# Performance work log

Measured on AMD Instinct MI355X. Metric: run time of the kernel, lower is better.

The kernel has to match this reference:

```python
import jax, jax.numpy as jnp
from jax import lax
import numpy as np

B, C_IN, DIMS, NW = 8, 64, 64, 8
T, H, W = 16, 56, 56
HID = C_IN // 4 + 1
EPS = 1e-5


def setup_inputs() -> dict:
    key = jax.random.key(0)
    ks = jax.random.split(key, 8)
    fan_in = C_IN * 27
    x = jax.random.normal(ks[0], (B, C_IN, T, H, W), dtype=jnp.float32)
    weights = jax.random.normal(ks[1], (NW, DIMS, C_IN, 3, 3, 3), dtype=jnp.float32) * np.sqrt(2.0 / fan_in)
    biases = jax.random.normal(ks[2], (NW, DIMS), dtype=jnp.float32)
    W1 = jax.random.normal(ks[3], (HID, C_IN), dtype=jnp.float32) * np.sqrt(1.0 / C_IN)
    b1 = jnp.zeros((HID,), dtype=jnp.float32)
    W2 = jax.random.normal(ks[4], (NW, HID), dtype=jnp.float32) * np.sqrt(1.0 / HID)
    b2 = jnp.zeros((NW,), dtype=jnp.float32)
    gamma = jnp.ones((DIMS,), dtype=jnp.float32)
    beta = jnp.zeros((DIMS,), dtype=jnp.float32)
    return {"x": x, "weights": weights, "biases": biases, "W1": W1, "b1": b1,
            "W2": W2, "b2": b2, "gamma": gamma, "beta": beta, "epochs_num": 5}


def reference(x, weights, biases, W1, b1, W2, b2, gamma, beta, epochs_num):
    # temperature schedule (epochs_num is a Python int)
    tau = 30.0 - 2.9 * epochs_num if epochs_num < 10 else 1.0
    # global max pool over (T,H,W) -> (B, C_in); sum over singleton dims is identity
    pooled = jnp.max(x, axis=(2, 3, 4))
    h = jax.nn.relu(pooled @ W1.T + b1)
    logits = h @ W2.T + b2
    phi = jax.nn.softmax(logits / tau, axis=1)  # (B, NW)
    # synthesize per-sample kernels and biases
    dyn_w = jnp.einsum('bn,noidhw->boidhw', phi, weights)  # (B, DIMS, C_in, 3,3,3)
    dyn_b = phi @ biases  # (B, DIMS)
    # per-sample conv3d (equivalent to grouped conv with groups=B)
    def conv1(xi, wi):
        return lax.conv_general_dilated(
            xi[None], wi, window_strides=(1, 1, 1), padding='SAME',
            dimension_numbers=('NCDHW', 'OIDHW', 'NCDHW'))[0]
    y = jax.vmap(conv1)(x, dyn_w) + dyn_b[:, :, None, None, None]
    # BatchNorm3d (training mode: batch statistics, biased var) + ReLU
    mean = jnp.mean(y, axis=(0, 2, 3, 4))
    var = jnp.var(y, axis=(0, 2, 3, 4))
    yn = (y - mean[None, :, None, None, None]) * lax.rsqrt(var + EPS)[None, :, None, None, None]
    yn = yn * gamma[None, :, None, None, None] + beta[None, :, None, None, None]
    return jax.nn.relu(yn)
```

## Files before the change

### kernel.cpp

```cpp
#include <hip/hip_runtime.h>
#include <hip/hip_bf16.h>

#define B_   8
#define CIN  64
#define DIMS 64
#define NW   8
#define T_   16
#define H_   56
#define W_   56
#define HID  17
#define THW  (T_*H_*W_)
#define HW   (H_*W_)
#define NPC  401408
#define EPS  1e-5f
#define PROWS 348

typedef __bf16 bf16x8 __attribute__((ext_vector_type(8)));
typedef float f32x4 __attribute__((ext_vector_type(4)));

#define OFF_XT     0
#define OFF_AT     51380224
#define OFF_POOLED 53149696
#define OFF_CHSUM  53151744
#define OFF_CHSQ   53152000
#define OFF_PHI    53152256
#define OFF_DYNB   53152512
#define OFF_SCALE  53154560
#define OFF_SHIFT  53154816
#define OFF_Y      53155072
#define WS_NEED_BF16Y (OFF_Y + 51380224)

__device__ __forceinline__ unsigned short f2bf(float f) {
    unsigned int u = __float_as_uint(f);
    u += 0x7fffu + ((u >> 16) & 1u);
    return (unsigned short)(u >> 16);
}
__device__ __forceinline__ float bf2f(unsigned short u) {
    return __uint_as_float(((unsigned int)u) << 16);
}
__device__ __forceinline__ unsigned int fenc(float f) {
    unsigned int b = __float_as_uint(f);
    return (b & 0x80000000u) ? ~b : (b | 0x80000000u);
}
__device__ __forceinline__ float fdec(unsigned int e) {
    return (e & 0x80000000u) ? __uint_as_float(e & 0x7fffffffu) : __uint_as_float(~e);
}

__device__ __forceinline__ float waveRedSum(float v) {
    #pragma unroll
    for (int o = 32; o > 0; o >>= 1) v += __shfl_down(v, o);
    return v;
}

__global__ __launch_bounds__(256) void xpose_kernel(const float* __restrict__ x,
                                                    unsigned short* __restrict__ xT,
                                                    unsigned int* __restrict__ pooled_u) {
    __shared__ float tile[CIN * W_];
    const int h = blockIdx.x, t = blockIdx.y, b = blockIdx.z;
    const int tid = threadIdx.x;
    {
        const int w = tid & 63, cg = tid >> 6;
        if (w < W_) {
            const size_t base = ((size_t)(b * CIN) * T_ + t) * HW + h * W_ + w;
            #pragma unroll
            for (int k = 0; k < 16; ++k) {
                const int c = cg * 16 + k;
                tile[c * W_ + w] = x[base + (size_t)c * (T_ * HW)];
            }
        }
    }
    __syncthreads();
    {
        const int w = tid >> 2, cq = tid & 3;
        if (w < W_) {
            unsigned int pk[8];
            #pragma unroll
            for (int kk = 0; kk < 8; ++kk) {
                const float f0 = tile[(cq * 16 + kk * 2) * W_ + w];
                const float f1 = tile[(cq * 16 + kk * 2 + 1) * W_ + w];
                pk[kk] = (unsigned int)f2bf(f0) | ((unsigned int)f2bf(f1) << 16);
            }
            unsigned short* dst = xT + ((((size_t)b * T_ + t) * H_ + h) * W_ + w) * CIN + cq * 16;
            *reinterpret_cast<uint4*>(dst)     = make_uint4(pk[0], pk[1], pk[2], pk[3]);
            *reinterpret_cast<uint4*>(dst + 8) = make_uint4(pk[4], pk[5], pk[6], pk[7]);
        }
    }
    if (tid < CIN) {
        float m = -3.4e38f;
        #pragma unroll 8
        for (int w = 0; w < W_; ++w) m = fmaxf(m, tile[tid * W_ + w]);
        atomicMax(&pooled_u[b * CIN + tid], fenc(m));
    }
}

__global__ __launch_bounds__(256) void mlp_kernel(const unsigned int* __restrict__ pooled_u,
                                                  const float* __restrict__ W1,
                                                  const float* __restrict__ b1,
                                                  const float* __restrict__ W2,
                                                  const float* __restrict__ b2,
                                                  const float* __restrict__ biases,
                                                  const void* __restrict__ epochs,
                                                  float* __restrict__ phi_out,
                                                  float* __restrict__ dynb) {
    __shared__ float pool_s[B_ * CIN];
    __shared__ float h_s[B_ * HID];
    __shared__ float lg_s[B_ * NW];
    __shared__ float phi_s[B_ * NW];
    const int tid = threadIdx.x;
    for (int i = tid; i < B_ * CIN; i += 256) pool_s[i] = fdec(pooled_u[i]);
    __syncthreads();
    if (tid < B_ * HID) {
        const int bb = tid / HID, j = tid % HID;
        float acc = b1[j];
        #pragma unroll
        for (int c = 0; c < CIN; ++c) acc += pool_s[bb * CIN + c] * W1[j * CIN + c];
        h_s[tid] = fmaxf(acc, 0.0f);
    }
    __syncthreads();
    if (tid < B_ * NW) {
        const int bb = tid >> 3, n = tid & 7;
        float acc = b2[n];
        #pragma unroll
        for (int j = 0; j < HID; ++j) acc += h_s[bb * HID + j] * W2[n * HID + j];
        lg_s[tid] = acc;
    }
    __syncthreads();
    if (tid < B_) {
        int e = ((const int*)epochs)[0];
        if (e < 0 || e > 1000000) e = (int)(((const float*)epochs)[0]);
        const float tau = (e < 10) ? (30.0f - 2.9f * (float)e) : 1.0f;
        float mx = -3.4e38f;
        #pragma unroll
        for (int n = 0; n < NW; ++n) mx = fmaxf(mx, lg_s[tid * NW + n]);
        float ex[NW], s = 0.0f;
        #pragma unroll
        for (int n = 0; n < NW; ++n) { ex[n] = expf((lg_s[tid * NW + n] - mx) / tau); s += ex[n]; }
        const bool ok = (s >= 1.0f) && (s < 1e37f);
        const float inv = ok ? (1.0f / s) : 0.0f;
        #pragma unroll
        for (int n = 0; n < NW; ++n) phi_s[tid * NW + n] = ok ? (ex[n] * inv) : 0.125f;
    }
    __syncthreads();
    if (tid < B_ * NW) phi_out[tid] = phi_s[tid];
    for (int idx = tid; idx < B_ * DIMS; idx += 256) {
        const int bb = idx >> 6, o = idx & 63;
        float a = 0.0f;
        #pragma unroll
        for (int n = 0; n < NW; ++n) a += phi_s[bb * NW + n] * biases[n * DIMS + o];
        dynb[idx] = a;
    }
}

__global__ __launch_bounds__(256) void awgen_kernel(const float* __restrict__ weights,
                                                    const float* __restrict__ phi,
                                                    unsigned short* __restrict__ At2) {
    const int b = blockIdx.x >> 5, oc = blockIdx.x & 31;
    const int o0 = oc * 2;
    __shared__ float ph[NW];
    if (threadIdx.x < NW) ph[threadIdx.x] = phi[b * NW + threadIdx.x];
    __syncthreads();
    const float4* w4 = reinterpret_cast<const float4*>(weights);
    for (int j = threadIdx.x; j < 864; j += 256) {
        f32x4 a = (f32x4){0.f, 0.f, 0.f, 0.f};
        #pragma unroll
        for (int n = 0; n < NW; ++n) {
            const float4 wv = w4[(size_t)(n * 64 + o0) * 432 + j];
            a[0] += ph[n] * wv.x;
            a[1] += ph[n] * wv.y;
            a[2] += ph[n] * wv.z;
            a[3] += ph[n] * wv.w;
        }
        #pragma unroll
        for (int k = 0; k < 4; ++k) {
            const int idx = j * 4 + k;
            const int oo = idx / 1728;
            const int rem = idx - oo * 1728;
            const int i = rem / 27;
            const int tap = rem - i * 27;
            const int o = o0 + oo;
            const int m = o >> 4, colv = o & 15;
            const int ks = i >> 5, kgv = (i >> 3) & 3, jj = i & 7;
            const size_t dst = (size_t)(b * 27 + tap) * 4096
                             + ((((ks * 4 + m) * 64) + kgv * 16 + colv) * 8 + jj);
            At2[dst] = f2bf(a[k]);
        }
    }
}

template<int BF16Y>
__global__ __launch_bounds__(256) void conv_kernel(const unsigned short* __restrict__ xT,
                                                   const unsigned short* __restrict__ At2,
                                                   const float* __restrict__ dynb,
                                                   float* __restrict__ yf,
                                                   unsigned short* __restrict__ yb) {
    __shared__ __align__(16) unsigned char xs[PROWS * 128];
    const int swz = (blockIdx.x & 7) * 224 + (blockIdx.x >> 3);
    const int b = swz / 224;
    const int rem = swz - b * 224;
    const int t = rem / 14, hg = rem - t * 14;
    const int tid = threadIdx.x;
    const int wave = tid >> 6, lane = tid & 63;
    const int col = lane & 15, kg = lane >> 4;
    const int hr = wave;
    const int h = hg * 4 + hr;

    for (int idx = tid; idx < PROWS * 8; idx += 256) {
        const int p = idx >> 3;
        const int hh = p / 58, ww = p - hh * 58;
        const int hha = hg * 4 + hh - 1;
        if (hha < 0 || hha >= H_ || ww == 0 || ww == 57)
            *reinterpret_cast<uint4*>(&xs[idx * 16]) = make_uint4(0u, 0u, 0u, 0u);
    }

    f32x4 acc[4][4];
    #pragma unroll
    for (int m = 0; m < 4; ++m)
        #pragma unroll
        for (int n = 0; n < 4; ++n) acc[m][n] = (f32x4){0.f, 0.f, 0.f, 0.f};

    const int sub = lane >> 3, q = lane & 7;

    for (int kd = 0; kd < 3; ++kd) {
        const int td = t + kd - 1;
        if (td < 0 || td >= T_) continue;
        __syncthreads();
        for (int item = wave; item < 42; item += 4) {
            const int hh = item / 7, qv = item - hh * 7;
            const int hha = hg * 4 + hh - 1;
            if (hha < 0 || hha >= H_) continue;
            const int p0 = hh * 58 + 1 + qv * 8;
            const int p = p0 + sub;
            const int w = qv * 8 + sub;
            const int qq = q ^ (p & 7);
            const unsigned short* src = xT
                + ((((size_t)b * T_ + td) * H_ + hha) * W_ + w) * CIN + qq * 8;
            __builtin_amdgcn_global_load_lds(
                (const __attribute__((address_space(1))) unsigned int*)(const void*)src,
                (__attribute__((address_space(3))) unsigned int*)(void*)&xs[p0 * 128],
                16, 0, 0);
        }
        asm volatile("s_waitcnt vmcnt(0)" ::: "memory");
        __syncthreads();
        #pragma unroll
        for (int kh = 0; kh < 3; ++kh) {
            #pragma unroll
            for (int kw = 0; kw < 3; ++kw) {
                const int tap = kd * 9 + kh * 3 + kw;
                const unsigned short* ap = At2 + (size_t)(b * 27 + tap) * 4096;
                bf16x8 afr[4][2], bfr[4][2];
                #pragma unroll
                for (int ks = 0; ks < 2; ++ks)
                    #pragma unroll
                    for (int m = 0; m < 4; ++m)
                        afr[m][ks] = *reinterpret_cast<const bf16x8*>(
                            ap + (((ks * 4 + m) * 64) + lane) * 8);
                #pragma unroll
                for (int n = 0; n < 4; ++n) {
                    int ww = n * 16 + col + kw;
                    if (ww > 57) ww = 57;
                    const int p = (hr + kh) * 58 + ww;
                    #pragma unroll
                    for (int ks = 0; ks < 2; ++ks) {
                        const int slot = (ks * 4 + kg) ^ (p & 7);
                        bfr[n][ks] = *reinterpret_cast<const bf16x8*>(&xs[p * 128 + slot * 16]);
                    }
                }
                #pragma unroll
                for (int ks = 0; ks < 2; ++ks)
                    #pragma unroll
                    for (int m = 0; m < 4; ++m)
                        #pragma unroll
                        for (int n = 0; n < 4; ++n)
                            acc[m][n] = __builtin_amdgcn_mfma_f32_16x16x32_bf16(
                                afr[m][ks], bfr[n][ks], acc[m][n], 0, 0, 0);
            }
        }
    }

    #pragma unroll
    for (int m = 0; m < 4; ++m) {
        #pragma unroll
        for (int r = 0; r < 4; ++r) {
            const int o = m * 16 + kg * 4 + r;
            const float db = dynb[b * DIMS + o];
            const size_t base = ((size_t)(b * DIMS + o) * T_ + t) * HW + h * W_;
            #pragma unroll
            for (int n = 0; n < 4; ++n) {
                const int w = n * 16 + col;
                if (w < W_) {
                    const float v = acc[m][n][r] + db;
                    if (BF16Y) yb[base + w] = f2bf(v);
                    else       yf[base + w] = v;
                }
            }
        }
    }
}

__global__ __launch_bounds__(256) void stats_f32_kernel(const float* __restrict__ y,
                                                        float* __restrict__ chsum,
                                                        float* __restrict__ chsq) {
    const int bo = blockIdx.x;
    const int o = bo & 63;
    const float4* src = reinterpret_cast<const float4*>(y + (size_t)bo * THW);
    float s = 0.0f, qq = 0.0f;
    for (int idx = threadIdx.x; idx < THW / 4; idx += 256) {
        float4 v = src[idx];
        s += v.x + v.y + v.z + v.w;
        qq += v.x * v.x + v.y * v.y + v.z * v.z + v.w * v.w;
    }
    s = waveRedSum(s);
    qq = waveRedSum(qq);
    __shared__ float ls[4], lq[4];
    const int wave = threadIdx.x >> 6, lane = threadIdx.x & 63;
    if (lane == 0) { ls[wave] = s; lq[wave] = qq; }
    __syncthreads();
    if (threadIdx.x == 0) {
        atomicAdd(&chsum[o], ls[0] + ls[1] + ls[2] + ls[3]);
        atomicAdd(&chsq[o],  lq[0] + lq[1] + lq[2] + lq[3]);
    }
}

__global__ __launch_bounds__(256) void stats_bf16_kernel(const unsigned short* __restrict__ yb,
                                                         float* __restrict__ chsum,
                                                         float* __restrict__ chsq) {
    const int bo = blockIdx.x;
    const int o = bo & 63;
    const uint4* src = reinterpret_cast<const uint4*>(yb + (size_t)bo * THW);
    float s = 0.0f, qq = 0.0f;
    for (int idx = threadIdx.x; idx < THW / 8; idx += 256) {
        uint4 v = src[idx];
        unsigned int vv[4] = {v.x, v.y, v.z, v.w};
        #pragma unroll
        for (int k = 0; k < 4; ++k) {
            float f0 = __uint_as_float((vv[k] & 0xffffu) << 16);
            float f1 = __uint_as_float(vv[k] & 0xffff0000u);
            s += f0 + f1;
            qq += f0 * f0 + f1 * f1;
        }
    }
    s = waveRedSum(s);
    qq = waveRedSum(qq);
    __shared__ float ls[4], lq[4];
    const int wave = threadIdx.x >> 6, lane = threadIdx.x & 63;
    if (lane == 0) { ls[wave] = s; lq[wave] = qq; }
    __syncthreads();
    if (threadIdx.x == 0) {
        atomicAdd(&chsum[o], ls[0] + ls[1] + ls[2] + ls[3]);
        atomicAdd(&chsq[o],  lq[0] + lq[1] + lq[2] + lq[3]);
    }
}

__global__ void fin_kernel(const float* __restrict__ chsum, const float* __restrict__ chsq,
                           const float* __restrict__ gamma, const float* __restrict__ beta,
                           float* __restrict__ scale, float* __restrict__ shift,
                           const unsigned int* __restrict__ pooled_u,
                           const float* __restrict__ phi,
                           int hostflags, float* __restrict__ out) {
    const int o = threadIdx.x;
    if (o < DIMS) {
        const float inv = 1.0f / (float)NPC;
        const float mean = chsum[o] * inv;
        const float var = chsq[o] * inv - mean * mean;
        const bool ok = (fabsf(mean) < 1e30f) && (var >= 0.0f) && (var < 1e30f);
        const float rstd = ok ? rsqrtf(var + EPS) : 0.0f;
        const float s = gamma[o] * rstd;
        scale[o] = ok ? s : 0.0f;
        shift[o] = ok ? (beta[o] - mean * s) : 0.69f;
    }
    if (o == 0) {
        int D = 32;
        const float p0 = fdec(pooled_u[0]);
        if (isfinite(p0) && fabsf(p0) > 1e-20f) D += 16;
        float sp = 0.0f, mp = 0.0f;
        for (int n = 0; n < NW; ++n) { sp += phi[n]; mp = fmaxf(mp, phi[n]); }
        if (fabsf(sp - 1.0f) < 0.01f) D += 32;
        float sq = 0.0f;
        for (int c = 0; c < DIMS; ++c) sq += chsq[c];
        if (sq > 1e-10f) D += 128;
        if (mp > 0.25f) D += 256;
        D += hostflags;
        if (D != 32 + 16 + 32 + 128) out[0] = (float)D;
    }
}

__global__ __launch_bounds__(256) void norm_f32_kernel(float* __restrict__ y,
                                                       const float* __restrict__ scale,
                                                       const float* __restrict__ shift) {
    const int bo = blockIdx.x >> 2, qq = blockIdx.x & 3;
    const int o = bo & 63;
    const float s = scale[o], sh = shift[o];
    float4* buf = reinterpret_cast<float4*>(y + (size_t)bo * THW) + qq * (THW / 16);
    for (int idx = threadIdx.x; idx < THW / 16; idx += 256) {
        float4 v = buf[idx];
        v.x = fmaxf(v.x * s + sh, 0.0f);
        v.y = fmaxf(v.y * s + sh, 0.0f);
        v.z = fmaxf(v.z * s + sh, 0.0f);
        v.w = fmaxf(v.w * s + sh, 0.0f);
        buf[idx] = v;
    }
}

__global__ __launch_bounds__(256) void norm_bf16_kernel(const unsigned short* __restrict__ yb,
                                                        const float* __restrict__ scale,
                                                        const float* __restrict__ shift,
                                                        float* __restrict__ out) {
    const int bo = blockIdx.x >> 2, qq = blockIdx.x & 3;
    const int o = bo & 63;
    const float s = scale[o], sh = shift[o];
    const uint4* src = reinterpret_cast<const uint4*>(yb + (size_t)bo * THW) + qq * (THW / 32);
    float4* dst = reinterpret_cast<float4*>(out + (size_t)bo * THW) + qq * (THW / 16);
    for (int idx = threadIdx.x; idx < THW / 32; idx += 256) {
        uint4 v = src[idx];
        unsigned int vv[4] = {v.x, v.y, v.z, v.w};
        float4 r0, r1;
        float* rp[2] = {&r0.x, &r1.x};
        #pragma unroll
        for (int k = 0; k < 4; ++k) {
            float f0 = __uint_as_float((vv[k] & 0xffffu) << 16);
            float f1 = __uint_as_float(vv[k] & 0xffff0000u);
            rp[k >> 1][(k & 1) * 2]     = fmaxf(f0 * s + sh, 0.0f);
            rp[k >> 1][(k & 1) * 2 + 1] = fmaxf(f1 * s + sh, 0.0f);
        }
        dst[idx * 2]     = r0;
        dst[idx * 2 + 1] = r1;
    }
}

extern "C" void kernel_launch(void* const* d_in, const int* in_sizes, int n_in,
                              void* d_out, int out_size, void* d_ws, size_t ws_size,
                              hipStream_t stream) {
    const float* x       = (const float*)d_in[0];
    const float* weights = (const float*)d_in[1];
    const float* biases  = (const float*)d_in[2];
    const float* W1      = (const float*)d_in[3];
    const float* b1      = (const float*)d_in[4];
    const float* W2      = (const float*)d_in[5];
    const float* b2      = (const float*)d_in[6];
    const float* gamma   = (const float*)d_in[7];
    const float* beta    = (const float*)d_in[8];
    const void*  epochs  = (const void*)d_in[9];

    float* out = (float*)d_out;
    char* ws = (char*)d_ws;
    unsigned short* xT   = (unsigned short*)(ws + OFF_XT);
    unsigned short* At2  = (unsigned short*)(ws + OFF_AT);
    unsigned int* pooled = (unsigned int*)(ws + OFF_POOLED);
    float* chsum  = (float*)(ws + OFF_CHSUM);
    float* chsq   = (float*)(ws + OFF_CHSQ);
    float* phi    = (float*)(ws + OFF_PHI);
    float* dynb   = (float*)(ws + OFF_DYNB);
    float* scale  = (float*)(ws + OFF_SCALE);
    float* shift  = (float*)(ws + OFF_SHIFT);
    unsigned short* ybf  = (unsigned short*)(ws + OFF_Y);

    const bool bf16y = (ws_size >= (size_t)WS_NEED_BF16Y);

    int hflags = 0;
    {
        const int expect[10] = {25690112, 884736, 512, 1088, 17, 136, 8, 64, 64, 1};
        if (n_in != 10) hflags |= 512;
        else {
            for (int i = 0; i < 10; ++i)
                if (in_sizes[i] != expect[i]) { hflags |= 512; break; }
        }
        if (out_size != 25690112) hflags |= 1024;
        if (ws_size < 53155072) hflags |= 2048;
    }

    hipMemsetAsync(ws + OFF_POOLED, 0, 2560, stream);

    xpose_kernel<<<dim3(H_, T_, B_), 256, 0, stream>>>(x, xT, pooled);
    mlp_kernel<<<1, 256, 0, stream>>>(pooled, W1, b1, W2, b2, biases, epochs, phi, dynb);
    awgen_kernel<<<256, 256, 0, stream>>>(weights, phi, At2);
    if (bf16y) {
        conv_kernel<1><<<1792, 256, 0, stream>>>(xT, At2, dynb, out, ybf);
        stats_bf16_kernel<<<B_ * DIMS, 256, 0, stream>>>(ybf, chsum, chsq);
        fin_kernel<<<1, 64, 0, stream>>>(chsum, chsq, gamma, beta, scale, shift,
                                         pooled, phi, hflags, out);
        norm_bf16_kernel<<<2048, 256, 0, stream>>>(ybf, scale, shift, out);
    } else {
        conv_kernel<0><<<1792, 256, 0, stream>>>(xT, At2, dynb, out, nullptr);
        stats_f32_kernel<<<B_ * DIMS, 256, 0, stream>>>(out, chsum, chsq);
        fin_kernel<<<1, 64, 0, stream>>>(chsum, chsq, gamma, beta, scale, shift,
                                         pooled, phi, hflags, out);
        norm_f32_kernel<<<2048, 256, 0, stream>>>(out, scale, shift);
    }
}
```

Baseline: 235.2 us.

## Split conv tiles along width into two halves to double block count

The conv kernel's output tile is halved along W: each block now covers 4 rows × 28 columns instead of the full 56-wide row, and the grid doubles to 3584 blocks. The shared-memory halo shrinks to 34-wide rows, the padding logic is reworked, and block-to-batch mapping changes so the batch index comes from the low bits. The goal is better load balance and occupancy on the GPU's compute units, using less LDS per block. In exchange, each block loads more halo per output and reuses each A-fragment load for half as many MFMAs, which adds weight-fetch traffic.

```diff
diff --git a/kernel.cpp b/kernel.cpp
--- a/kernel.cpp
+++ b/kernel.cpp
@@ -13,7 +13,8 @@
 #define HW   (H_*W_)
 #define NPC  401408
 #define EPS  1e-5f
-#define PROWS 348
+#define WWID 34
+#define PROWS_W (6*WWID)
 
 typedef __bf16 bf16x8 __attribute__((ext_vector_type(8)));
 typedef float f32x4 __attribute__((ext_vector_type(4)));
@@ -193,53 +194,57 @@
                                                    const float* __restrict__ dynb,
                                                    float* __restrict__ yf,
                                                    unsigned short* __restrict__ yb) {
-    __shared__ __align__(16) unsigned char xs[PROWS * 128];
-    const int swz = (blockIdx.x & 7) * 224 + (blockIdx.x >> 3);
-    const int b = swz / 224;
-    const int rem = swz - b * 224;
-    const int t = rem / 14, hg = rem - t * 14;
+    __shared__ __align__(16) unsigned char xs[PROWS_W * 128];
+    const int b = blockIdx.x & 7;
+    const int rem = blockIdx.x >> 3;
+    const int t = rem / 28;
+    const int r2 = rem - t * 28;
+    const int hg = r2 >> 1, wb = r2 & 1;
     const int tid = threadIdx.x;
     const int wave = tid >> 6, lane = tid & 63;
     const int col = lane & 15, kg = lane >> 4;
     const int hr = wave;
     const int h = hg * 4 + hr;
 
-    for (int idx = tid; idx < PROWS * 8; idx += 256) {
-        const int p = idx >> 3;
-        const int hh = p / 58, ww = p - hh * 58;
-        const int hha = hg * 4 + hh - 1;
-        if (hha < 0 || hha >= H_ || ww == 0 || ww == 57)
-            *reinterpret_cast<uint4*>(&xs[idx * 16]) = make_uint4(0u, 0u, 0u, 0u);
-    }
-
-    f32x4 acc[4][4];
+    for (int idx = tid; idx < PROWS_W * 8; idx += 256)
+        *reinterpret_cast<uint4*>(&xs[idx * 16]) = make_uint4(0u, 0u, 0u, 0u);
+
+    f32x4 acc[4][2];
     #pragma unroll
     for (int m = 0; m < 4; ++m)
         #pragma unroll
-        for (int n = 0; n < 4; ++n) acc[m][n] = (f32x4){0.f, 0.f, 0.f, 0.f};
+        for (int n = 0; n < 2; ++n) acc[m][n] = (f32x4){0.f, 0.f, 0.f, 0.f};
 
     const int sub = lane >> 3, q = lane & 7;
+    const int ww_s = (wb == 0) ? 1 : 0;
 
     for (int kd = 0; kd < 3; ++kd) {
         const int td = t + kd - 1;
         if (td < 0 || td >= T_) continue;
         __syncthreads();
-        for (int item = wave; item < 42; item += 4) {
-            const int hh = item / 7, qv = item - hh * 7;
+        for (int item = wave; item < 24; item += 4) {
+            const int hh = item >> 2, qv = item & 3;
             const int hha = hg * 4 + hh - 1;
             if (hha < 0 || hha >= H_) continue;
-            const int p0 = hh * 58 + 1 + qv * 8;
+            const int p0 = hh * WWID + ww_s + qv * 8;
             const int p = p0 + sub;
-            const int w = qv * 8 + sub;
+            const int ww = ww_s + qv * 8 + sub;
+            int w_in = wb * 28 + ww - 1;
+            if (w_in > 55) w_in = 55;
             const int qq = q ^ (p & 7);
             const unsigned short* src = xT
-                + ((((size_t)b * T_ + td) * H_ + hha) * W_ + w) * CIN + qq * 8;
+                + ((((size_t)b * T_ + td) * H_ + hha) * W_ + w_in) * CIN + qq * 8;
             __builtin_amdgcn_global_load_lds(
                 (const __attribute__((address_space(1))) unsigned int*)(const void*)src,
                 (__attribute__((address_space(3))) unsigned int*)(void*)&xs[p0 * 128],
                 16, 0, 0);
         }
         asm volatile("s_waitcnt vmcnt(0)" ::: "memory");
+        if (wb && wave == 3 && lane < 48) {
+            const int hh = lane >> 3, qz = lane & 7;
+            *reinterpret_cast<uint4*>(&xs[(hh * WWID + 29) * 128 + qz * 16]) =
+                make_uint4(0u, 0u, 0u, 0u);
+        }
         __syncthreads();
         #pragma unroll
         for (int kh = 0; kh < 3; ++kh) {
@@ -247,7 +252,7 @@
             for (int kw = 0; kw < 3; ++kw) {
                 const int tap = kd * 9 + kh * 3 + kw;
                 const unsigned short* ap = At2 + (size_t)(b * 27 + tap) * 4096;
-                bf16x8 afr[4][2], bfr[4][2];
+                bf16x8 afr[4][2], bfr[2][2];
                 #pragma unroll
                 for (int ks = 0; ks < 2; ++ks)
                     #pragma unroll
@@ -255,10 +260,10 @@
                         afr[m][ks] = *reinterpret_cast<const bf16x8*>(
                             ap + (((ks * 4 + m) * 64) + lane) * 8);
                 #pragma unroll
-                for (int n = 0; n < 4; ++n) {
+                for (int n = 0; n < 2; ++n) {
                     int ww = n * 16 + col + kw;
-                    if (ww > 57) ww = 57;
-                    const int p = (hr + kh) * 58 + ww;
+                    if (ww > 29) ww = 29;
+                    const int p = (hr + kh) * WWID + ww;
                     #pragma unroll
                     for (int ks = 0; ks < 2; ++ks) {
                         const int slot = (ks * 4 + kg) ^ (p & 7);
@@ -270,7 +275,7 @@
                     #pragma unroll
                     for (int m = 0; m < 4; ++m)
                         #pragma unroll
-                        for (int n = 0; n < 4; ++n)
+                        for (int n = 0; n < 2; ++n)
                             acc[m][n] = __builtin_amdgcn_mfma_f32_16x16x32_bf16(
                                 afr[m][ks], bfr[n][ks], acc[m][n], 0, 0, 0);
             }
@@ -283,14 +288,14 @@
         for (int r = 0; r < 4; ++r) {
             const int o = m * 16 + kg * 4 + r;
             const float db = dynb[b * DIMS + o];
-            const size_t base = ((size_t)(b * DIMS + o) * T_ + t) * HW + h * W_;
+            const size_t base = ((size_t)(b * DIMS + o) * T_ + t) * HW + h * W_ + wb * 28;
             #pragma unroll
-            for (int n = 0; n < 4; ++n) {
-                const int w = n * 16 + col;
-                if (w < W_) {
+            for (int n = 0; n < 2; ++n) {
+                const int wc = n * 16 + col;
+                if (wc < 28) {
                     const float v = acc[m][n][r] + db;
-                    if (BF16Y) yb[base + w] = f2bf(v);
-                    else       yf[base + w] = v;
+                    if (BF16Y) yb[base + wc] = f2bf(v);
+                    else       yf[base + wc] = v;
                 }
             }
         }
@@ -474,13 +479,13 @@
     mlp_kernel<<<1, 256, 0, stream>>>(pooled, W1, b1, W2, b2, biases, epochs, phi, dynb);
     awgen_kernel<<<256, 256, 0, stream>>>(weights, phi, At2);
     if (bf16y) {
-        conv_kernel<1><<<1792, 256, 0, stream>>>(xT, At2, dynb, out, ybf);
+        conv_kernel<1><<<3584, 256, 0, stream>>>(xT, At2, dynb, out, ybf);
         stats_bf16_kernel<<<B_ * DIMS, 256, 0, stream>>>(ybf, chsum, chsq);
         fin_kernel<<<1, 64, 0, stream>>>(chsum, chsq, gamma, beta, scale, shift,
                                          pooled, phi, hflags, out);
         norm_bf16_kernel<<<2048, 256, 0, stream>>>(ybf, scale, shift, out);
     } else {
-        conv_kernel<0><<<1792, 256, 0, stream>>>(xT, At2, dynb, out, nullptr);
+        conv_kernel<0><<<3584, 256, 0, stream>>>(xT, At2, dynb, out, nullptr);
         stats_f32_kernel<<<B_ * DIMS, 256, 0, stream>>>(out, chsum, chsq);
         fin_kernel<<<1, 64, 0, stream>>>(chsum, chsq, gamma, beta, scale, shift,
                                          pooled, phi, hflags, out);
```

New measurement: 268.2 us. 14.1% more time.
